# Kernel optimization log

Hardware: AMD Instinct MI355X
Metric: run time of the kernel (lower is better)

Reference implementation:

```python
import jax, jax.numpy as jnp
import numpy as np

WINDOW = 7
DIM = 384
HEADS = 12
HEAD_DIM = DIM // HEADS
SCALE = HEAD_DIM ** -0.5
N = WINDOW * WINDOW  # 49 tokens per window


def _rel_pos_index():
    coords = np.stack(np.meshgrid(np.arange(WINDOW), np.arange(WINDOW), indexing='ij'))  # [2, W, W]
    flat = coords.reshape(2, -1)  # [2, N]
    rel = flat[:, :, None] - flat[:, None, :]  # [2, N, N]
    rel = rel.transpose(1, 2, 0).copy()  # [N, N, 2]
    rel[:, :, 0] += WINDOW - 1
    rel[:, :, 1] += WINDOW - 1
    rel[:, :, 0] *= 2 * WINDOW - 1
    return jnp.asarray(rel.sum(-1).reshape(-1), dtype=jnp.int32)  # [N*N]


def setup_inputs() -> dict:
    key = jax.random.key(0)
    k1, k2, k3, k4, k5 = jax.random.split(key, 5)
    B = 4096
    x = jax.random.normal(k1, (B, N, DIM), dtype=jnp.float32)
    w_qkv = jax.random.normal(k2, (DIM, 3 * DIM), dtype=jnp.float32) * (DIM ** -0.5)
    w_proj = jax.random.normal(k3, (DIM, DIM), dtype=jnp.float32) * (DIM ** -0.5)
    b_proj = jax.random.normal(k4, (DIM,), dtype=jnp.float32) * 0.01
    bias_table = jax.random.normal(k5, ((2 * WINDOW - 1) ** 2, HEADS), dtype=jnp.float32) * 0.02
    return {"x": x, "w_qkv": w_qkv, "w_proj": w_proj, "b_proj": b_proj,
            "bias_table": bias_table, "rel_pos_index": _rel_pos_index()}


def reference(x, w_qkv, w_proj, b_proj, bias_table, rel_pos_index):
    B, n, C = x.shape
    qkv = (x @ w_qkv).reshape(B, n, 3, HEADS, HEAD_DIM)
    q, k, v = [jnp.transpose(qkv[:, :, i], (0, 2, 1, 3)) for i in range(3)]  # [B, H, N, D]
    attn = jnp.einsum('bhnd,bhmd->bhnm', q, k) * SCALE
    bias = bias_table[rel_pos_index].reshape(n, n, HEADS)  # [N, N, H]
    attn = attn + jnp.transpose(bias, (2, 0, 1))[None]  # broadcast over batch
    # quadratic normalization (use_poly=True): replaces softmax
    attn = attn * attn
    attn = attn / (attn.sum(axis=-1, keepdims=True) + 1e-6)
    out = jnp.einsum('bhnm,bhmd->bhnd', attn, v)
    out = jnp.transpose(out, (0, 2, 1, 3)).reshape(B, n, C)
    return out @ w_proj + b_proj
```

## Files before the change

kernel.cpp:

```cpp
#include <hip/hip_runtime.h>


using s16x8 = __attribute__((ext_vector_type(8))) short;
using f32x4 = __attribute__((ext_vector_type(4))) float;

#define AS1 __attribute__((address_space(1)))
#define AS3 __attribute__((address_space(3)))

__device__ __forceinline__ short f2bf(float f) {
  unsigned int u = __float_as_uint(f);
  u += 0x7fffu + ((u >> 16) & 1u);
  return (short)(u >> 16);
}

__device__ __forceinline__ void load16_to_lds(const void* g, void* l) {
  __builtin_amdgcn_global_load_lds((AS1 void*)(void*)g, (AS3 void*)l, 16, 0, 0);
}

__global__ __launch_bounds__(256) void convert_x(const float* __restrict__ x,
                                                 short* __restrict__ xb) {
  int i = blockIdx.x * 256 + threadIdx.x;
  const float4* xv = (const float4*)x;
  float4 a = xv[2 * i];
  float4 c = xv[2 * i + 1];
  s16x8 o;
  o[0] = f2bf(a.x); o[1] = f2bf(a.y); o[2] = f2bf(a.z); o[3] = f2bf(a.w);
  o[4] = f2bf(c.x); o[5] = f2bf(c.y); o[6] = f2bf(c.z); o[7] = f2bf(c.w);
  ((s16x8*)xb)[i] = o;
}

__global__ __launch_bounds__(256) void prep(const float* __restrict__ wqkv,
                                            const float* __restrict__ wproj,
                                            const float* __restrict__ btab,
                                            const int* __restrict__ rel,
                                            short* __restrict__ wqt,
                                            short* __restrict__ wpt,
                                            float* __restrict__ bini) {
  int i = blockIdx.x * 256 + threadIdx.x;
  if (i < 442368) {
    int c = i / 384, kx = i - c * 384;
    wqt[i] = f2bf(wqkv[kx * 1152 + c]);
  } else if (i < 442368 + 147456) {
    int j = i - 442368;
    int c = j / 384, kx = j - c * 384;
    wpt[j] = f2bf(wproj[kx * 384 + c]);
  } else if (i < 442368 + 147456 + 49152) {
    int j = i - (442368 + 147456);
    int head = j >> 12;
    int rem = j & 4095;
    int fi = rem >> 10; int rem2 = rem & 1023;
    int fj = rem2 >> 8; int rem3 = rem2 & 255;
    int l = rem3 >> 2;  int r = rem3 & 3;
    int row = fi * 16 + (l >> 4) * 4 + r;
    int col = fj * 16 + (l & 15);
    float val = 0.f;
    if (row < 49 && col < 49)
      val = btab[rel[row * 49 + col] * 12 + head] * 5.656854249492381f;
    bini[j] = val;
  }
}

__global__ __launch_bounds__(256) void gemm_qkv(const short* __restrict__ A,
                                                const short* __restrict__ Bt,
                                                short* __restrict__ q,
                                                short* __restrict__ k,
                                                short* __restrict__ v) {
  __shared__ __align__(16) short As[2][128 * 32];
  __shared__ __align__(16) short Bs[2][128 * 32];
  const int t = threadIdx.x;
  const int wave = t >> 6, lane = t & 63;
  const int quad = lane >> 4, l15 = lane & 15;
  const int wm = wave & 1, wn = wave >> 1;
  const int m0 = blockIdx.y * 128;
  const int n0 = blockIdx.x * 128;

  auto stage = [&](int buf, int kt) {
#pragma unroll
    for (int p = 0; p < 2; ++p) {
      int o = p * 4096 + wave * 1024 + lane * 16;
      int row = o >> 6, colb = o & 63;
      load16_to_lds((const char*)A + (size_t)(m0 + row) * 768 + kt * 64 + colb,
                    (char*)(&As[buf][0]) + o);
      load16_to_lds((const char*)Bt + (size_t)(n0 + row) * 768 + kt * 64 + colb,
                    (char*)(&Bs[buf][0]) + o);
    }
  };

  f32x4 acc[4][4] = {};
  stage(0, 0);
  for (int kt = 0; kt < 12; ++kt) {
    __syncthreads();
    if (kt + 1 < 12) stage((kt + 1) & 1, kt + 1);
    const short* as = &As[kt & 1][0];
    const short* bs = &Bs[kt & 1][0];
    s16x8 af[4], bfr[4];
#pragma unroll
    for (int i = 0; i < 4; ++i)
      af[i] = *(const s16x8*)(as + (wm * 64 + i * 16 + l15) * 32 + quad * 8);
#pragma unroll
    for (int j = 0; j < 4; ++j)
      bfr[j] = *(const s16x8*)(bs + (wn * 64 + j * 16 + l15) * 32 + quad * 8);
#pragma unroll
    for (int i = 0; i < 4; ++i)
#pragma unroll
      for (int j = 0; j < 4; ++j)
        acc[i][j] = __builtin_amdgcn_mfma_f32_16x16x32_bf16(af[i], bfr[j], acc[i][j], 0, 0, 0);
  }

  const int part = n0 / 384;
  short* dst = (part == 0) ? q : ((part == 1) ? k : v);
  const int cb = (n0 - part * 384) + wn * 64 + l15;
#pragma unroll
  for (int i = 0; i < 4; ++i) {
#pragma unroll
    for (int r = 0; r < 4; ++r) {
      int m = m0 + wm * 64 + i * 16 + quad * 4 + r;
      int b = m / 49;
      int n = m - b * 49;
      int base = b * 18816 + n * 32;
#pragma unroll
      for (int j = 0; j < 4; ++j) {
        int c = cb + j * 16;
        int h = c >> 5, d = c & 31;
        dst[base + h * 1568 + d] = f2bf(acc[i][j][r]);
      }
    }
  }
}

__global__ __launch_bounds__(256) void attn(const short* __restrict__ q,
                                            const short* __restrict__ k,
                                            const short* __restrict__ v,
                                            const float* __restrict__ biasinit,
                                            short* __restrict__ O) {
  __shared__ __align__(16) short smem[4 * 6912];
  const int t = threadIdx.x, wave = t >> 6, lane = t & 63;
  const int quad = lane >> 4, l15 = lane & 15;
  const int wid = blockIdx.x;
  const int b = wid / 3;
  const int head = (wid - 3 * b) * 4 + wave;
  short* VT = smem + wave * 6912;
  short* P = VT + 2304;
  const size_t hb = ((size_t)b * 12 + head) * 1568;
  const short* qh = q + hb;
  const short* kh = k + hb;
  const short* vh = v + hb;

  f32x4 acc[4][4];
  const float* bi = biasinit + head * 4096;
#pragma unroll
  for (int i = 0; i < 4; ++i)
#pragma unroll
    for (int j = 0; j < 4; ++j)
      acc[i][j] = *(const f32x4*)(bi + (i * 4 + j) * 256 + lane * 4);

  for (int e = lane; e < 512; e += 64) {
    int d = e >> 4, n = 49 + (e & 15);
    VT[d * 72 + n] = 0;
  }
  for (int e = lane; e < 1568; e += 64) {
    int n = e >> 5, d = e & 31;
    VT[d * 72 + n] = vh[e];
  }

  s16x8 aq[4], bk[4];
#pragma unroll
  for (int i = 0; i < 4; ++i)
    aq[i] = *(const s16x8*)(qh + (i * 16 + l15) * 32 + quad * 8);
#pragma unroll
  for (int j = 0; j < 4; ++j)
    bk[j] = *(const s16x8*)(kh + (j * 16 + l15) * 32 + quad * 8);
#pragma unroll
  for (int i = 0; i < 4; ++i)
#pragma unroll
    for (int j = 0; j < 4; ++j)
      acc[i][j] = __builtin_amdgcn_mfma_f32_16x16x32_bf16(aq[i], bk[j], acc[i][j], 0, 0, 0);

  const float SC = 0.17677669529663687f;
  float inv[4][4];
#pragma unroll
  for (int i = 0; i < 4; ++i) {
#pragma unroll
    for (int r = 0; r < 4; ++r) {
      int row = i * 16 + quad * 4 + r;
      float rs = 0.f;
#pragma unroll
      for (int j = 0; j < 4; ++j) {
        int col = j * 16 + l15;
        float s = acc[i][j][r] * SC;
        float p = s * s;
        p = (col < 49) ? p : 0.f;
        rs += p;
        P[row * 72 + col] = f2bf(p);
      }
      rs += __shfl_xor(rs, 1);
      rs += __shfl_xor(rs, 2);
      rs += __shfl_xor(rs, 4);
      rs += __shfl_xor(rs, 8);
      inv[i][r] = 1.0f / (rs + 1e-6f);
    }
  }

  s16x8 bvf[2][2];
#pragma unroll
  for (int nn = 0; nn < 2; ++nn)
#pragma unroll
    for (int kk = 0; kk < 2; ++kk)
      bvf[nn][kk] = *(const s16x8*)(VT + (nn * 16 + l15) * 72 + kk * 32 + quad * 8);
  f32x4 oa[4][2] = {};
#pragma unroll
  for (int i = 0; i < 4; ++i)
#pragma unroll
    for (int kk = 0; kk < 2; ++kk) {
      s16x8 ap = *(const s16x8*)(P + (i * 16 + l15) * 72 + kk * 32 + quad * 8);
#pragma unroll
      for (int nn = 0; nn < 2; ++nn)
        oa[i][nn] = __builtin_amdgcn_mfma_f32_16x16x32_bf16(ap, bvf[nn][kk], oa[i][nn], 0, 0, 0);
    }

  const size_t obase = (size_t)b * 49 * 384 + head * 32;
#pragma unroll
  for (int i = 0; i < 4; ++i)
#pragma unroll
    for (int r = 0; r < 4; ++r) {
      int n = i * 16 + quad * 4 + r;
      if (n < 49) {
#pragma unroll
        for (int nn = 0; nn < 2; ++nn) {
          float val = oa[i][nn][r] * inv[i][r];
          O[obase + (size_t)n * 384 + nn * 16 + l15] = f2bf(val);
        }
      }
    }
}

__global__ __launch_bounds__(256) void gemm_proj(const short* __restrict__ A,
                                                 const short* __restrict__ Bt,
                                                 const float* __restrict__ bias,
                                                 float* __restrict__ out) {
  __shared__ __align__(16) short As[2][128 * 32];
  __shared__ __align__(16) short Bs[2][128 * 32];
  const int t = threadIdx.x;
  const int wave = t >> 6, lane = t & 63;
  const int quad = lane >> 4, l15 = lane & 15;
  const int wm = wave & 1, wn = wave >> 1;
  const int m0 = blockIdx.y * 128;
  const int n0 = blockIdx.x * 128;

  auto stage = [&](int buf, int kt) {
#pragma unroll
    for (int p = 0; p < 2; ++p) {
      int o = p * 4096 + wave * 1024 + lane * 16;
      int row = o >> 6, colb = o & 63;
      load16_to_lds((const char*)A + (size_t)(m0 + row) * 768 + kt * 64 + colb,
                    (char*)(&As[buf][0]) + o);
      load16_to_lds((const char*)Bt + (size_t)(n0 + row) * 768 + kt * 64 + colb,
                    (char*)(&Bs[buf][0]) + o);
    }
  };

  f32x4 acc[4][4] = {};
  stage(0, 0);
  for (int kt = 0; kt < 12; ++kt) {
    __syncthreads();
    if (kt + 1 < 12) stage((kt + 1) & 1, kt + 1);
    const short* as = &As[kt & 1][0];
    const short* bs = &Bs[kt & 1][0];
    s16x8 af[4], bfr[4];
#pragma unroll
    for (int i = 0; i < 4; ++i)
      af[i] = *(const s16x8*)(as + (wm * 64 + i * 16 + l15) * 32 + quad * 8);
#pragma unroll
    for (int j = 0; j < 4; ++j)
      bfr[j] = *(const s16x8*)(bs + (wn * 64 + j * 16 + l15) * 32 + quad * 8);
#pragma unroll
    for (int i = 0; i < 4; ++i)
#pragma unroll
      for (int j = 0; j < 4; ++j)
        acc[i][j] = __builtin_amdgcn_mfma_f32_16x16x32_bf16(af[i], bfr[j], acc[i][j], 0, 0, 0);
  }

  const int cb = n0 + wn * 64 + l15;
  float bj[4];
#pragma unroll
  for (int j = 0; j < 4; ++j) bj[j] = bias[cb + j * 16];
#pragma unroll
  for (int i = 0; i < 4; ++i) {
#pragma unroll
    for (int r = 0; r < 4; ++r) {
      int m = m0 + wm * 64 + i * 16 + quad * 4 + r;
      float* orow = out + (size_t)m * 384;
#pragma unroll
      for (int j = 0; j < 4; ++j)
        orow[cb + j * 16] = acc[i][j][r] + bj[j];
    }
  }
}

extern "C" void kernel_launch(void* const* d_in, const int* in_sizes, int n_in,
                              void* d_out, int out_size, void* d_ws, size_t ws_size,
                              hipStream_t stream) {
  const float* x      = (const float*)d_in[0];
  const float* w_qkv  = (const float*)d_in[1];
  const float* w_proj = (const float*)d_in[2];
  const float* b_proj = (const float*)d_in[3];
  const float* btab   = (const float*)d_in[4];
  const int*   rel    = (const int*)d_in[5];

  char* ws = (char*)d_ws;
  short* xb   = (short*)(ws);
  short* q    = (short*)(ws + 154140672);
  short* k    = (short*)(ws + 308281344);
  short* v    = (short*)(ws + 462422016);
  short* wqt  = (short*)(ws + 616562688);
  short* wpt  = (short*)(ws + 617447424);
  float* bini = (float*)(ws + 617742336);

  convert_x<<<37632, 256, 0, stream>>>(x, xb);
  prep<<<2496, 256, 0, stream>>>(w_qkv, w_proj, btab, rel, wqt, wpt, bini);
  gemm_qkv<<<dim3(9, 1568), 256, 0, stream>>>(xb, wqt, q, k, v);
  attn<<<12288, 256, 0, stream>>>(q, k, v, bini, xb);
  gemm_proj<<<dim3(3, 1568), 256, 0, stream>>>(xb, wpt, b_proj, (float*)d_out);
}
```

Baseline: 1.208 ms.

## Fuse conversion, QKV GEMM, window attention and projection into one per-window kernel

Replaces the four-kernel pipeline (x conversion, QKV GEMM, attention, projection GEMM) with one kernel that runs one 49-token window per 512-thread block. The x-to-bf16 conversion happens on load, and Q, K, V, P and the attention output all stay in about 160KB of dynamic LDS. This removes the large global round trips of the bf16 copy of x and of the q/k/v/attention-output tensors. In exchange, each block streams the full transposed weight matrices straight from global/L2 into registers without LDS staging. Occupancy drops to one large block per CU, and the attention phase spreads 12 heads over 8 waves, which leaves the waves unevenly loaded.

```diff
diff --git a/kernel.cpp b/kernel.cpp
--- a/kernel.cpp
+++ b/kernel.cpp
@@ -2,10 +2,8 @@
 
 
 using s16x8 = __attribute__((ext_vector_type(8))) short;
+using u16x4 = __attribute__((ext_vector_type(4))) unsigned short;
 using f32x4 = __attribute__((ext_vector_type(4))) float;
-
-#define AS1 __attribute__((address_space(1)))
-#define AS3 __attribute__((address_space(3)))
 
 __device__ __forceinline__ short f2bf(float f) {
   unsigned int u = __float_as_uint(f);
@@ -13,21 +11,12 @@
   return (short)(u >> 16);
 }
 
-__device__ __forceinline__ void load16_to_lds(const void* g, void* l) {
-  __builtin_amdgcn_global_load_lds((AS1 void*)(void*)g, (AS3 void*)l, 16, 0, 0);
-}
-
-__global__ __launch_bounds__(256) void convert_x(const float* __restrict__ x,
-                                                 short* __restrict__ xb) {
-  int i = blockIdx.x * 256 + threadIdx.x;
-  const float4* xv = (const float4*)x;
-  float4 a = xv[2 * i];
-  float4 c = xv[2 * i + 1];
-  s16x8 o;
-  o[0] = f2bf(a.x); o[1] = f2bf(a.y); o[2] = f2bf(a.z); o[3] = f2bf(a.w);
-  o[4] = f2bf(c.x); o[5] = f2bf(c.y); o[6] = f2bf(c.z); o[7] = f2bf(c.w);
-  ((s16x8*)xb)[i] = o;
-}
+#define LDS_X    0
+#define LDS_Q    37632
+#define LDS_K    75264
+#define LDS_V    112896
+#define LDS_ZERO 162048
+#define LDS_TOTAL 162064
 
 __global__ __launch_bounds__(256) void prep(const float* __restrict__ wqkv,
                                             const float* __restrict__ wproj,
@@ -60,241 +49,206 @@
   }
 }
 
-__global__ __launch_bounds__(256) void gemm_qkv(const short* __restrict__ A,
-                                                const short* __restrict__ Bt,
-                                                short* __restrict__ q,
-                                                short* __restrict__ k,
-                                                short* __restrict__ v) {
-  __shared__ __align__(16) short As[2][128 * 32];
-  __shared__ __align__(16) short Bs[2][128 * 32];
+__global__ __launch_bounds__(512, 2) void fused_win(const float* __restrict__ x,
+                                                    const short* __restrict__ wqt,
+                                                    const short* __restrict__ wpt,
+                                                    const float* __restrict__ bias_proj,
+                                                    const float* __restrict__ bini,
+                                                    float* __restrict__ out) {
+  extern __shared__ char smem[];
   const int t = threadIdx.x;
-  const int wave = t >> 6, lane = t & 63;
-  const int quad = lane >> 4, l15 = lane & 15;
-  const int wm = wave & 1, wn = wave >> 1;
-  const int m0 = blockIdx.y * 128;
-  const int n0 = blockIdx.x * 128;
-
-  auto stage = [&](int buf, int kt) {
-#pragma unroll
-    for (int p = 0; p < 2; ++p) {
-      int o = p * 4096 + wave * 1024 + lane * 16;
-      int row = o >> 6, colb = o & 63;
-      load16_to_lds((const char*)A + (size_t)(m0 + row) * 768 + kt * 64 + colb,
-                    (char*)(&As[buf][0]) + o);
-      load16_to_lds((const char*)Bt + (size_t)(n0 + row) * 768 + kt * 64 + colb,
-                    (char*)(&Bs[buf][0]) + o);
-    }
-  };
-
-  f32x4 acc[4][4] = {};
-  stage(0, 0);
+  const int wave = t >> 6, lane = t & 63, quad = lane >> 4, l15 = lane & 15;
+  const size_t xbase = (size_t)blockIdx.x * (49 * 384);
+
+  for (int task = t; task < 2352; task += 512) {
+    int r = task / 48, c = task - r * 48;
+    const float4* src = (const float4*)(x + xbase + r * 384 + c * 8);
+    float4 a = src[0], b = src[1];
+    s16x8 o;
+    o[0] = f2bf(a.x); o[1] = f2bf(a.y); o[2] = f2bf(a.z); o[3] = f2bf(a.w);
+    o[4] = f2bf(b.x); o[5] = f2bf(b.y); o[6] = f2bf(b.z); o[7] = f2bf(b.w);
+    *(s16x8*)(smem + (c * 49 + r) * 16) = o;
+  }
+  if (t < 8) ((short*)(smem + LDS_ZERO))[t] = 0;
+  __syncthreads();
+
+  const int colbase = wave * 48;
+  for (int p = 0; p < 3; ++p) {
+    f32x4 acc[4][3] = {};
+    const short* bsrc = wqt + (size_t)(p * 384 + colbase) * 384;
+    for (int kt = 0; kt < 12; ++kt) {
+      s16x8 af[4], bfr[3];
+      const int cb = (kt * 4 + quad) * 784;
+#pragma unroll
+      for (int i = 0; i < 4; ++i) {
+        int row = i * 16 + l15;
+        af[i] = *(const s16x8*)(smem + ((row < 49) ? (cb + row * 16) : LDS_ZERO));
+      }
+#pragma unroll
+      for (int j = 0; j < 3; ++j)
+        bfr[j] = *(const s16x8*)(bsrc + (j * 16 + l15) * 384 + kt * 32 + quad * 8);
+#pragma unroll
+      for (int i = 0; i < 4; ++i)
+#pragma unroll
+        for (int j = 0; j < 3; ++j)
+          acc[i][j] = __builtin_amdgcn_mfma_f32_16x16x32_bf16(af[i], bfr[j], acc[i][j], 0, 0, 0);
+    }
+    if (p < 2) {
+      char* reg = smem + ((p == 0) ? LDS_Q : LDS_K);
+#pragma unroll
+      for (int j = 0; j < 3; ++j) {
+        int gcol = colbase + j * 16 + l15;
+        char* base = reg + (gcol >> 3) * 784 + (gcol & 7) * 2;
+#pragma unroll
+        for (int i = 0; i < 4; ++i)
+#pragma unroll
+          for (int r = 0; r < 4; ++r) {
+            int tok = i * 16 + quad * 4 + r;
+            if (tok < 49) *(short*)(base + tok * 16) = f2bf(acc[i][j][r]);
+          }
+      }
+    } else {
+#pragma unroll
+      for (int j = 0; j < 3; ++j) {
+        int gcol = colbase + j * 16 + l15;
+        int h = gcol >> 5, dd = gcol & 31;
+#pragma unroll
+        for (int i = 0; i < 4; ++i) {
+          u16x4 pk;
+          pk[0] = (unsigned short)f2bf(acc[i][j][0]);
+          pk[1] = (unsigned short)f2bf(acc[i][j][1]);
+          pk[2] = (unsigned short)f2bf(acc[i][j][2]);
+          pk[3] = (unsigned short)f2bf(acc[i][j][3]);
+          int chunk = h * 8 + i * 2 + (quad >> 1);
+          *(u16x4*)(smem + LDS_V + (chunk * 32 + dd) * 16 + (quad & 1) * 8) = pk;
+        }
+      }
+    }
+  }
+  __syncthreads();
+
+  const float SC = 0.17677669529663687f;
+  char* pbase = smem + wave * 3136;
+  for (int h = wave; h < 12; h += 8) {
+    const float* bi = bini + h * 4096 + lane * 4;
+    f32x4 sacc[4][4];
+#pragma unroll
+    for (int i = 0; i < 4; ++i)
+#pragma unroll
+      for (int j = 0; j < 4; ++j)
+        sacc[i][j] = *(const f32x4*)(bi + (i * 4 + j) * 256);
+
+    const int qoff = LDS_Q + (h * 4 + quad) * 784;
+    const int koff = LDS_K + (h * 4 + quad) * 784;
+    s16x8 aq[4], bk[4];
+#pragma unroll
+    for (int i = 0; i < 4; ++i) {
+      int row = i * 16 + l15;
+      aq[i] = *(const s16x8*)(smem + ((row < 49) ? (qoff + row * 16) : LDS_ZERO));
+      bk[i] = *(const s16x8*)(smem + ((row < 49) ? (koff + row * 16) : LDS_ZERO));
+    }
+#pragma unroll
+    for (int i = 0; i < 4; ++i)
+#pragma unroll
+      for (int j = 0; j < 4; ++j)
+        sacc[i][j] = __builtin_amdgcn_mfma_f32_16x16x32_bf16(aq[i], bk[j], sacc[i][j], 0, 0, 0);
+
+    float rs[4][4];
+#pragma unroll
+    for (int i = 0; i < 4; ++i)
+#pragma unroll
+      for (int r = 0; r < 4; ++r) rs[i][r] = 0.f;
+
+    f32x4 oa[4][2] = {};
+#pragma unroll
+    for (int half = 0; half < 2; ++half) {
+#pragma unroll
+      for (int jj = 0; jj < 2; ++jj) {
+        int j = half * 2 + jj;
+#pragma unroll
+        for (int i = 0; i < 4; ++i)
+#pragma unroll
+          for (int r = 0; r < 4; ++r) {
+            int tok = i * 16 + quad * 4 + r;
+            float s = sacc[i][j][r] * SC;
+            float pp = s * s;
+            rs[i][r] += pp;
+            if (tok < 49)
+              *(short*)(pbase + ((jj * 2 + (l15 >> 3)) * 49 + tok) * 16 + (l15 & 7) * 2) = f2bf(pp);
+          }
+      }
+#pragma unroll
+      for (int i = 0; i < 4; ++i) {
+        int row = i * 16 + l15;
+        s16x8 ap = *(const s16x8*)((row < 49) ? (pbase + (quad * 49 + row) * 16)
+                                              : (smem + LDS_ZERO));
+#pragma unroll
+        for (int nn = 0; nn < 2; ++nn) {
+          s16x8 bv = *(const s16x8*)(smem + LDS_V +
+                       ((h * 8 + half * 4 + quad) * 32 + nn * 16 + l15) * 16);
+          oa[i][nn] = __builtin_amdgcn_mfma_f32_16x16x32_bf16(ap, bv, oa[i][nn], 0, 0, 0);
+        }
+      }
+    }
+#pragma unroll
+    for (int i = 0; i < 4; ++i)
+#pragma unroll
+      for (int r = 0; r < 4; ++r) {
+        float v = rs[i][r];
+        v += __shfl_xor(v, 1);
+        v += __shfl_xor(v, 2);
+        v += __shfl_xor(v, 4);
+        v += __shfl_xor(v, 8);
+        rs[i][r] = 1.0f / (v + 1e-6f);
+      }
+#pragma unroll
+    for (int nn = 0; nn < 2; ++nn) {
+      char* obase = smem + LDS_Q + (h * 4 + nn * 2 + (l15 >> 3)) * 784 + (l15 & 7) * 2;
+#pragma unroll
+      for (int i = 0; i < 4; ++i)
+#pragma unroll
+        for (int r = 0; r < 4; ++r) {
+          int tok = i * 16 + quad * 4 + r;
+          if (tok < 49) *(short*)(obase + tok * 16) = f2bf(oa[i][nn][r] * rs[i][r]);
+        }
+    }
+  }
+  __syncthreads();
+
+  f32x4 pacc[4][3] = {};
+  const short* bsrc = wpt + (size_t)colbase * 384;
   for (int kt = 0; kt < 12; ++kt) {
-    __syncthreads();
-    if (kt + 1 < 12) stage((kt + 1) & 1, kt + 1);
-    const short* as = &As[kt & 1][0];
-    const short* bs = &Bs[kt & 1][0];
-    s16x8 af[4], bfr[4];
-#pragma unroll
-    for (int i = 0; i < 4; ++i)
-      af[i] = *(const s16x8*)(as + (wm * 64 + i * 16 + l15) * 32 + quad * 8);
-#pragma unroll
-    for (int j = 0; j < 4; ++j)
-      bfr[j] = *(const s16x8*)(bs + (wn * 64 + j * 16 + l15) * 32 + quad * 8);
-#pragma unroll
-    for (int i = 0; i < 4; ++i)
-#pragma unroll
-      for (int j = 0; j < 4; ++j)
-        acc[i][j] = __builtin_amdgcn_mfma_f32_16x16x32_bf16(af[i], bfr[j], acc[i][j], 0, 0, 0);
-  }
-
-  const int part = n0 / 384;
-  short* dst = (part == 0) ? q : ((part == 1) ? k : v);
-  const int cb = (n0 - part * 384) + wn * 64 + l15;
-#pragma unroll
-  for (int i = 0; i < 4; ++i) {
+    s16x8 af[4], bfr[3];
+    const int cb = LDS_Q + (kt * 4 + quad) * 784;
+#pragma unroll
+    for (int i = 0; i < 4; ++i) {
+      int row = i * 16 + l15;
+      af[i] = *(const s16x8*)(smem + ((row < 49) ? (cb + row * 16) : LDS_ZERO));
+    }
+#pragma unroll
+    for (int j = 0; j < 3; ++j)
+      bfr[j] = *(const s16x8*)(bsrc + (j * 16 + l15) * 384 + kt * 32 + quad * 8);
+#pragma unroll
+    for (int i = 0; i < 4; ++i)
+#pragma unroll
+      for (int j = 0; j < 3; ++j)
+        pacc[i][j] = __builtin_amdgcn_mfma_f32_16x16x32_bf16(af[i], bfr[j], pacc[i][j], 0, 0, 0);
+  }
+  float bj[3];
+#pragma unroll
+  for (int j = 0; j < 3; ++j) bj[j] = bias_proj[colbase + j * 16 + l15];
+#pragma unroll
+  for (int i = 0; i < 4; ++i)
 #pragma unroll
     for (int r = 0; r < 4; ++r) {
-      int m = m0 + wm * 64 + i * 16 + quad * 4 + r;
-      int b = m / 49;
-      int n = m - b * 49;
-      int base = b * 18816 + n * 32;
-#pragma unroll
-      for (int j = 0; j < 4; ++j) {
-        int c = cb + j * 16;
-        int h = c >> 5, d = c & 31;
-        dst[base + h * 1568 + d] = f2bf(acc[i][j][r]);
-      }
-    }
-  }
-}
-
-__global__ __launch_bounds__(256) void attn(const short* __restrict__ q,
-                                            const short* __restrict__ k,
-                                            const short* __restrict__ v,
-                                            const float* __restrict__ biasinit,
-                                            short* __restrict__ O) {
-  __shared__ __align__(16) short smem[4 * 6912];
-  const int t = threadIdx.x, wave = t >> 6, lane = t & 63;
-  const int quad = lane >> 4, l15 = lane & 15;
-  const int wid = blockIdx.x;
-  const int b = wid / 3;
-  const int head = (wid - 3 * b) * 4 + wave;
-  short* VT = smem + wave * 6912;
-  short* P = VT + 2304;
-  const size_t hb = ((size_t)b * 12 + head) * 1568;
-  const short* qh = q + hb;
-  const short* kh = k + hb;
-  const short* vh = v + hb;
-
-  f32x4 acc[4][4];
-  const float* bi = biasinit + head * 4096;
-#pragma unroll
-  for (int i = 0; i < 4; ++i)
-#pragma unroll
-    for (int j = 0; j < 4; ++j)
-      acc[i][j] = *(const f32x4*)(bi + (i * 4 + j) * 256 + lane * 4);
-
-  for (int e = lane; e < 512; e += 64) {
-    int d = e >> 4, n = 49 + (e & 15);
-    VT[d * 72 + n] = 0;
-  }
-  for (int e = lane; e < 1568; e += 64) {
-    int n = e >> 5, d = e & 31;
-    VT[d * 72 + n] = vh[e];
-  }
-
-  s16x8 aq[4], bk[4];
-#pragma unroll
-  for (int i = 0; i < 4; ++i)
-    aq[i] = *(const s16x8*)(qh + (i * 16 + l15) * 32 + quad * 8);
-#pragma unroll
-  for (int j = 0; j < 4; ++j)
-    bk[j] = *(const s16x8*)(kh + (j * 16 + l15) * 32 + quad * 8);
-#pragma unroll
-  for (int i = 0; i < 4; ++i)
-#pragma unroll
-    for (int j = 0; j < 4; ++j)
-      acc[i][j] = __builtin_amdgcn_mfma_f32_16x16x32_bf16(aq[i], bk[j], acc[i][j], 0, 0, 0);
-
-  const float SC = 0.17677669529663687f;
-  float inv[4][4];
-#pragma unroll
-  for (int i = 0; i < 4; ++i) {
-#pragma unroll
-    for (int r = 0; r < 4; ++r) {
-      int row = i * 16 + quad * 4 + r;
-      float rs = 0.f;
-#pragma unroll
-      for (int j = 0; j < 4; ++j) {
-        int col = j * 16 + l15;
-        float s = acc[i][j][r] * SC;
-        float p = s * s;
-        p = (col < 49) ? p : 0.f;
-        rs += p;
-        P[row * 72 + col] = f2bf(p);
-      }
-      rs += __shfl_xor(rs, 1);
-      rs += __shfl_xor(rs, 2);
-      rs += __shfl_xor(rs, 4);
-      rs += __shfl_xor(rs, 8);
-      inv[i][r] = 1.0f / (rs + 1e-6f);
-    }
-  }
-
-  s16x8 bvf[2][2];
-#pragma unroll
-  for (int nn = 0; nn < 2; ++nn)
-#pragma unroll
-    for (int kk = 0; kk < 2; ++kk)
-      bvf[nn][kk] = *(const s16x8*)(VT + (nn * 16 + l15) * 72 + kk * 32 + quad * 8);
-  f32x4 oa[4][2] = {};
-#pragma unroll
-  for (int i = 0; i < 4; ++i)
-#pragma unroll
-    for (int kk = 0; kk < 2; ++kk) {
-      s16x8 ap = *(const s16x8*)(P + (i * 16 + l15) * 72 + kk * 32 + quad * 8);
-#pragma unroll
-      for (int nn = 0; nn < 2; ++nn)
-        oa[i][nn] = __builtin_amdgcn_mfma_f32_16x16x32_bf16(ap, bvf[nn][kk], oa[i][nn], 0, 0, 0);
-    }
-
-  const size_t obase = (size_t)b * 49 * 384 + head * 32;
-#pragma unroll
-  for (int i = 0; i < 4; ++i)
-#pragma unroll
-    for (int r = 0; r < 4; ++r) {
-      int n = i * 16 + quad * 4 + r;
-      if (n < 49) {
-#pragma unroll
-        for (int nn = 0; nn < 2; ++nn) {
-          float val = oa[i][nn][r] * inv[i][r];
-          O[obase + (size_t)n * 384 + nn * 16 + l15] = f2bf(val);
-        }
-      }
-    }
-}
-
-__global__ __launch_bounds__(256) void gemm_proj(const short* __restrict__ A,
-                                                 const short* __restrict__ Bt,
-                                                 const float* __restrict__ bias,
-                                                 float* __restrict__ out) {
-  __shared__ __align__(16) short As[2][128 * 32];
-  __shared__ __align__(16) short Bs[2][128 * 32];
-  const int t = threadIdx.x;
-  const int wave = t >> 6, lane = t & 63;
-  const int quad = lane >> 4, l15 = lane & 15;
-  const int wm = wave & 1, wn = wave >> 1;
-  const int m0 = blockIdx.y * 128;
-  const int n0 = blockIdx.x * 128;
-
-  auto stage = [&](int buf, int kt) {
-#pragma unroll
-    for (int p = 0; p < 2; ++p) {
-      int o = p * 4096 + wave * 1024 + lane * 16;
-      int row = o >> 6, colb = o & 63;
-      load16_to_lds((const char*)A + (size_t)(m0 + row) * 768 + kt * 64 + colb,
-                    (char*)(&As[buf][0]) + o);
-      load16_to_lds((const char*)Bt + (size_t)(n0 + row) * 768 + kt * 64 + colb,
-                    (char*)(&Bs[buf][0]) + o);
-    }
-  };
-
-  f32x4 acc[4][4] = {};
-  stage(0, 0);
-  for (int kt = 0; kt < 12; ++kt) {
-    __syncthreads();
-    if (kt + 1 < 12) stage((kt + 1) & 1, kt + 1);
-    const short* as = &As[kt & 1][0];
-    const short* bs = &Bs[kt & 1][0];
-    s16x8 af[4], bfr[4];
-#pragma unroll
-    for (int i = 0; i < 4; ++i)
-      af[i] = *(const s16x8*)(as + (wm * 64 + i * 16 + l15) * 32 + quad * 8);
-#pragma unroll
-    for (int j = 0; j < 4; ++j)
-      bfr[j] = *(const s16x8*)(bs + (wn * 64 + j * 16 + l15) * 32 + quad * 8);
-#pragma unroll
-    for (int i = 0; i < 4; ++i)
-#pragma unroll
-      for (int j = 0; j < 4; ++j)
-        acc[i][j] = __builtin_amdgcn_mfma_f32_16x16x32_bf16(af[i], bfr[j], acc[i][j], 0, 0, 0);
-  }
-
-  const int cb = n0 + wn * 64 + l15;
-  float bj[4];
-#pragma unroll
-  for (int j = 0; j < 4; ++j) bj[j] = bias[cb + j * 16];
-#pragma unroll
-  for (int i = 0; i < 4; ++i) {
-#pragma unroll
-    for (int r = 0; r < 4; ++r) {
-      int m = m0 + wm * 64 + i * 16 + quad * 4 + r;
-      float* orow = out + (size_t)m * 384;
-#pragma unroll
-      for (int j = 0; j < 4; ++j)
-        orow[cb + j * 16] = acc[i][j][r] + bj[j];
-    }
-  }
+      int tok = i * 16 + quad * 4 + r;
+      if (tok < 49) {
+        float* orow = out + xbase + (size_t)tok * 384 + colbase + l15;
+#pragma unroll
+        for (int j = 0; j < 3; ++j)
+          orow[j * 16] = pacc[i][j][r] + bj[j];
+      }
+    }
 }
 
 extern "C" void kernel_launch(void* const* d_in, const int* in_sizes, int n_in,
@@ -308,17 +262,17 @@
   const int*   rel    = (const int*)d_in[5];
 
   char* ws = (char*)d_ws;
-  short* xb   = (short*)(ws);
-  short* q    = (short*)(ws + 154140672);
-  short* k    = (short*)(ws + 308281344);
-  short* v    = (short*)(ws + 462422016);
-  short* wqt  = (short*)(ws + 616562688);
-  short* wpt  = (short*)(ws + 617447424);
-  float* bini = (float*)(ws + 617742336);
-
-  convert_x<<<37632, 256, 0, stream>>>(x, xb);
+  short* wqt  = (short*)(ws);
+  short* wpt  = (short*)(ws + 884736);
+  float* bini = (float*)(ws + 1179648);
+
+  static int once = [] {
+    return (int)hipFuncSetAttribute((const void*)fused_win,
+                                    hipFuncAttributeMaxDynamicSharedMemorySize,
+                                    LDS_TOTAL);
+  }();
+  (void)once;
+
   prep<<<2496, 256, 0, stream>>>(w_qkv, w_proj, btab, rel, wqt, wpt, bini);
-  gemm_qkv<<<dim3(9, 1568), 256, 0, stream>>>(xb, wqt, q, k, v);
-  attn<<<12288, 256, 0, stream>>>(q, k, v, bini, xb);
-  gemm_proj<<<dim3(3, 1568), 256, 0, stream>>>(xb, wpt, b_proj, (float*)d_out);
-}
+  fused_win<<<4096, 512, LDS_TOTAL, stream>>>(x, wqt, wpt, b_proj, bini, (float*)d_out);
+}
```

New measurement: 1.158 ms. 4.1% less time.
